# Performance work log

Hardware: AMD Instinct MI355X
Metric: run time of the kernel (lower is better)

## Reference

```python
import jax, jax.numpy as jnp
import numpy as np

B, S, D, H = 2, 2048, 1024, 16
HD = D // H  # head depth


def setup_inputs() -> dict:
    key = jax.random.key(0)
    ks = jax.random.split(key, 8)
    scale = 0.02
    K = jax.random.normal(ks[0], (B, S, D), jnp.float32)
    V = jax.random.normal(ks[1], (B, S, D), jnp.float32)
    Q = jax.random.normal(ks[2], (B, S, D), jnp.float32)
    # causal additive mask: 1.0 where attention is disallowed (strict upper triangle)
    mask = jnp.broadcast_to(
        jnp.triu(jnp.ones((S, S), jnp.float32), k=1)[None, None, :, :], (B, 1, S, S)
    )
    Wk = jax.random.normal(ks[3], (D, D), jnp.float32) * scale
    Wv = jax.random.normal(ks[4], (D, D), jnp.float32) * scale
    Wq = jax.random.normal(ks[5], (D, D), jnp.float32) * scale
    Wo = jax.random.normal(ks[6], (D, D), jnp.float32) * scale
    z = jnp.zeros((D,), jnp.float32)
    return {"K": K, "V": V, "Q": Q, "mask": mask,
            "Wk": Wk, "bk": z, "Wv": Wv, "bv": z,
            "Wq": Wq, "bq": z, "Wo": Wo, "bo": z}


def _split_heads(x):  # [B,S,D] -> [B,H,S,HD]
    return x.reshape(B, S, H, HD).transpose(0, 2, 1, 3)


def reference(K, V, Q, mask, Wk, bk, Wv, bv, Wq, bq, Wo, bo):
    k = _split_heads(K @ Wk + bk)
    v = _split_heads(V @ Wv + bv)
    q = _split_heads(Q @ Wq + bq)
    # NOTE: source scales by sqrt(d_model), not sqrt(head_depth)
    logits = jnp.einsum("bhqd,bhkd->bhqk", q, k) / jnp.sqrt(jnp.float32(D))
    logits = logits + mask * (-1e9)
    attn = jax.nn.softmax(logits, axis=-1)
    out = jnp.einsum("bhqk,bhkd->bhqd", attn, v)  # [B,H,S,HD]
    out = out.transpose(0, 2, 1, 3).reshape(B, S, D)
    return out @ Wo + bo
```

## Files before the change

kernel.cpp:

```cpp
#include <hip/hip_runtime.h>
#include <hip/hip_bf16.h>

typedef unsigned short u16;
typedef unsigned int u32;
typedef unsigned long long u64;
typedef __attribute__((ext_vector_type(8))) __bf16 bf16x8;
typedef __attribute__((ext_vector_type(4))) float f32x4;

#define SEQ 2048
#define DM 1024
#define NH 16
#define HDim 64

__device__ __forceinline__ float bf_lo(u32 u) { return __uint_as_float(u << 16); }
__device__ __forceinline__ float bf_hi(u32 u) { return __uint_as_float(u & 0xffff0000u); }
__device__ __forceinline__ u16 f2bf(float f) {
    u32 u = __float_as_uint(f);
    u32 r = (u + 0x7fffu + ((u >> 16) & 1u)) >> 16;
    return (u16)r;
}
__device__ __forceinline__ float bf2f(u16 h) { return __uint_as_float(((u32)h) << 16); }

#define GLD16(g, l)                                                         \
    __builtin_amdgcn_global_load_lds(                                       \
        (const __attribute__((address_space(1))) void*)(g),                 \
        (__attribute__((address_space(3))) void*)(l), 16, 0, 0)

__global__ __launch_bounds__(64)
void detect_dtype(const u32* __restrict__ q, int* __restrict__ flag)
{
    const int t = threadIdx.x;
    const u32 w = q[t];
    const int e0 = ((w & 0xffffu) >> 7) & 0xff;
    const int e1 = ((w >> 16) >> 7) & 0xff;
    const int big = (e0 >= 0x90 || e1 >= 0x90) ? 1 : 0;
    const unsigned long long b = __ballot(big);
    if (t == 0) *flag = (b != 0ull) ? 1 : 0;
}

__global__ __launch_bounds__(256)
void prep_x(const void* __restrict__ q, const void* __restrict__ k,
            const void* __restrict__ v, u16* __restrict__ dst,
            const int* __restrict__ flagp)
{
    const int z = blockIdx.z;
    const void* src = (z == 0) ? q : (z == 1) ? k : v;
    const size_t i0 = ((size_t)blockIdx.x * 256 + threadIdx.x) * 8;
    u16* d = dst + (size_t)z * 4194304 + i0;
    if (*flagp) {
        const uint4* s = reinterpret_cast<const uint4*>((const float*)src + i0);
        uint4 a = s[0], b = s[1];
        u16 o[8];
        o[0] = f2bf(__uint_as_float(a.x)); o[1] = f2bf(__uint_as_float(a.y));
        o[2] = f2bf(__uint_as_float(a.z)); o[3] = f2bf(__uint_as_float(a.w));
        o[4] = f2bf(__uint_as_float(b.x)); o[5] = f2bf(__uint_as_float(b.y));
        o[6] = f2bf(__uint_as_float(b.z)); o[7] = f2bf(__uint_as_float(b.w));
        *reinterpret_cast<uint4*>(d) = *reinterpret_cast<const uint4*>(o);
    } else {
        *reinterpret_cast<uint4*>(d) =
            *reinterpret_cast<const uint4*>((const u16*)src + i0);
    }
}

__global__ __launch_bounds__(256)
void transpose_w(const void* __restrict__ w0, const void* __restrict__ w1,
                 const void* __restrict__ w2, const void* __restrict__ w3,
                 u16* __restrict__ wt, const int* __restrict__ flagp)
{
    __shared__ u16 T[64 * 66];
    const int z = blockIdx.z;
    const void* src = (z == 0) ? w0 : (z == 1) ? w1 : (z == 2) ? w2 : w3;
    const int n0 = blockIdx.x * 64, k0 = blockIdx.y * 64;
    const int t = threadIdx.x;
    const int c = t & 63, g = t >> 6;
    const int f = *flagp;
    if (f) {
        const float* W = (const float*)src;
#pragma unroll
        for (int i = 0; i < 16; i++) {
            const int kl = g * 16 + i;
            T[kl * 66 + c] = f2bf(W[(size_t)(k0 + kl) * DM + n0 + c]);
        }
    } else {
        const u16* W = (const u16*)src;
#pragma unroll
        for (int i = 0; i < 16; i++) {
            const int kl = g * 16 + i;
            T[kl * 66 + c] = W[(size_t)(k0 + kl) * DM + n0 + c];
        }
    }
    __syncthreads();
    u16* dst = wt + (size_t)z * 1048576;
#pragma unroll
    for (int i = 0; i < 16; i++) {
        const int nl = g * 16 + i;
        dst[(size_t)(n0 + nl) * DM + k0 + c] = T[c * 66 + nl];
    }
}

__global__ __launch_bounds__(256)
void prep_bias(const void* __restrict__ b0, const void* __restrict__ b1,
               const void* __restrict__ b2, const void* __restrict__ b3,
               u16* __restrict__ dst, const int* __restrict__ flagp)
{
    const int t = threadIdx.x;
    const int f = *flagp;
#pragma unroll
    for (int j = 0; j < 16; j++) {
        const int idx = t * 16 + j;
        const int z = idx >> 10, e = idx & 1023;
        const void* src = (z == 0) ? b0 : (z == 1) ? b1 : (z == 2) ? b2 : b3;
        dst[idx] = f ? f2bf(((const float*)src)[e]) : ((const u16*)src)[e];
    }
}

__global__ __launch_bounds__(256)
void gemm128(const u16* __restrict__ Xall, const u16* __restrict__ Wtall,
             const u16* __restrict__ ball, u16* __restrict__ Yall,
             void* __restrict__ dout, int zbase, const int* __restrict__ flagp)
{
    __shared__ __align__(16) u16 As[128 * 32];
    __shared__ __align__(16) u16 Bs[128 * 32];

    const int zz = zbase + blockIdx.z;
    const u16* X  = Xall + ((zz == 3) ? 0 : (size_t)zz * 4194304);
    const u16* Wt = Wtall + (size_t)zz * 1048576;

    const int t    = threadIdx.x;
    const int w    = t >> 6;
    const int lane = t & 63;
    const int quad = lane >> 4;
    const int ln   = lane & 15;
    const int m0   = blockIdx.y * 128;
    const int n0   = blockIdx.x * 128;

    f32x4 acc[4][4];
#pragma unroll
    for (int i = 0; i < 4; i++)
#pragma unroll
        for (int j = 0; j < 4; j++) acc[i][j] = (f32x4){0.f, 0.f, 0.f, 0.f};

    const u16* ag = X  + (size_t)(m0 + w * 32 + (lane >> 2)) * DM + (lane & 3) * 8;
    const u16* bg = Wt + (size_t)(n0 + w * 32 + (lane >> 2)) * DM + (lane & 3) * 8;
    u16* al = &As[w * 1024];
    u16* bl = &Bs[w * 1024];

    const int wr = (w >> 1) * 64;
    const int wc = (w & 1) * 64;

    for (int kk = 0; kk < DM; kk += 32) {
        GLD16(ag,             al);
        GLD16(ag + 16 * DM,   al + 512);
        GLD16(bg,             bl);
        GLD16(bg + 16 * DM,   bl + 512);
        ag += 32; bg += 32;
        __syncthreads();

        bf16x8 af[4], bfr[4];
#pragma unroll
        for (int rt = 0; rt < 4; rt++)
            af[rt] = *reinterpret_cast<const bf16x8*>(&As[(wr + rt * 16 + ln) * 32 + quad * 8]);
#pragma unroll
        for (int ct = 0; ct < 4; ct++)
            bfr[ct] = *reinterpret_cast<const bf16x8*>(&Bs[(wc + ct * 16 + ln) * 32 + quad * 8]);
#pragma unroll
        for (int rt = 0; rt < 4; rt++)
#pragma unroll
            for (int ct = 0; ct < 4; ct++)
                acc[rt][ct] = __builtin_amdgcn_mfma_f32_16x16x32_bf16(
                    af[rt], bfr[ct], acc[rt][ct], 0, 0, 0);
        __syncthreads();
    }

    const int f = *flagp;
    const float scale = (zz == 0) ? 0.03125f : 1.0f;
    u16* Y = Yall + (size_t)zz * 4194304;

#pragma unroll
    for (int ct = 0; ct < 4; ct++) {
        const int n = n0 + wc + ct * 16 + ln;
        const float bv = bf2f(ball[zz * 1024 + n]);
        const int h = n >> 6, hd = n & (HDim - 1);
#pragma unroll
        for (int rt = 0; rt < 4; rt++) {
            const int m = m0 + wr + rt * 16 + quad * 4;
            if (zz == 2) {
                const int b = m >> 11, s = m & (SEQ - 1);
                u16 o4[4];
#pragma unroll
                for (int r = 0; r < 4; r++) o4[r] = f2bf(acc[rt][ct][r] + bv);
                *reinterpret_cast<u64*>(
                    Y + (((size_t)(b * NH + h) * HDim + hd) * SEQ + s)) =
                    *reinterpret_cast<const u64*>(o4);
            } else if (zz == 3) {
#pragma unroll
                for (int r = 0; r < 4; r++) {
                    const float val = acc[rt][ct][r] + bv;
                    if (f) ((float*)dout)[(size_t)(m + r) * DM + n] = val;
                    else   ((u16*)dout)[(size_t)(m + r) * DM + n] = f2bf(val);
                }
            } else {
#pragma unroll
                for (int r = 0; r < 4; r++) {
                    const int mm = m + r;
                    const int b = mm >> 11, s = mm & (SEQ - 1);
                    Y[(((size_t)(b * NH + h)) * SEQ + s) * HDim + hd] =
                        f2bf((acc[rt][ct][r] + bv) * scale);
                }
            }
        }
    }
}

__global__ __launch_bounds__(256)
void attn_mfma(const u16* __restrict__ qh, const u16* __restrict__ kh,
               const u16* __restrict__ vt, u16* __restrict__ ctx)
{
    __shared__ __align__(16) u16 Ks[64 * 72];
    __shared__ __align__(16) u16 Vs[64 * 72];
    __shared__ __align__(16) u16 Ps[64 * 72];

    const int t    = threadIdx.x;
    const int qt   = blockIdx.x;
    const int bh   = blockIdx.y;
    const int w    = t >> 6;
    const int lane = t & 63;
    const int quad = lane >> 4;
    const int ln   = lane & 15;

    const size_t kbase = (size_t)bh * SEQ * HDim;
    const size_t vbase = (size_t)bh * HDim * SEQ;

    const u16* qrow = qh + kbase + (size_t)(qt * 64 + w * 16 + ln) * HDim;
    const bf16x8 qf0 = *reinterpret_cast<const bf16x8*>(qrow + quad * 8);
    const bf16x8 qf1 = *reinterpret_cast<const bf16x8*>(qrow + 32 + quad * 8);

    f32x4 o[4];
#pragma unroll
    for (int i = 0; i < 4; i++) o[i] = (f32x4){0.f, 0.f, 0.f, 0.f};
    float lsum[4] = {0.f, 0.f, 0.f, 0.f};

    const int srow = t >> 2;
    const int sc   = (t & 3) * 16;
    const int myrow = qt * 64 + w * 16 + quad * 4;
    const int ntiles = qt + 1;

    for (int kt = 0; kt < ntiles; kt++) {
        {
            const uint4* ks = reinterpret_cast<const uint4*>(
                kh + kbase + (size_t)(kt * 64 + srow) * HDim + sc);
            uint4* kd = reinterpret_cast<uint4*>(&Ks[srow * 72 + sc]);
            kd[0] = ks[0];
            kd[1] = ks[1];
            const uint4* vs = reinterpret_cast<const uint4*>(
                vt + vbase + (size_t)srow * SEQ + kt * 64 + sc);
            uint4* vd = reinterpret_cast<uint4*>(&Vs[srow * 72 + sc]);
            vd[0] = vs[0];
            vd[1] = vs[1];
        }
        __syncthreads();

        f32x4 s[4];
#pragma unroll
        for (int ct = 0; ct < 4; ct++) {
            const u16* kr = &Ks[(ct * 16 + ln) * 72 + quad * 8];
            bf16x8 kf0 = *reinterpret_cast<const bf16x8*>(kr);
            bf16x8 kf1 = *reinterpret_cast<const bf16x8*>(kr + 32);
            f32x4 z = (f32x4){0.f, 0.f, 0.f, 0.f};
            z = __builtin_amdgcn_mfma_f32_16x16x32_bf16(qf0, kf0, z, 0, 0, 0);
            s[ct] = __builtin_amdgcn_mfma_f32_16x16x32_bf16(qf1, kf1, z, 0, 0, 0);
        }

#pragma unroll
        for (int ct = 0; ct < 4; ct++) {
            const int kcol = kt * 64 + ct * 16 + ln;
#pragma unroll
            for (int r = 0; r < 4; r++) {
                const float e = (kcol <= myrow + r) ? __expf(s[ct][r]) : 0.f;
                lsum[r] += e;
                Ps[(w * 16 + quad * 4 + r) * 72 + ct * 16 + ln] = f2bf(e);
            }
        }

#pragma unroll
        for (int ks = 0; ks < 2; ks++) {
            bf16x8 pf = *reinterpret_cast<const bf16x8*>(
                &Ps[(w * 16 + ln) * 72 + ks * 32 + quad * 8]);
#pragma unroll
            for (int nt = 0; nt < 4; nt++) {
                bf16x8 vf = *reinterpret_cast<const bf16x8*>(
                    &Vs[(nt * 16 + ln) * 72 + ks * 32 + quad * 8]);
                o[nt] = __builtin_amdgcn_mfma_f32_16x16x32_bf16(pf, vf, o[nt], 0, 0, 0);
            }
        }
        __syncthreads();
    }

#pragma unroll
    for (int m = 1; m < 16; m <<= 1) {
#pragma unroll
        for (int r = 0; r < 4; r++) lsum[r] += __shfl_xor(lsum[r], m);
    }
    float inv[4];
#pragma unroll
    for (int r = 0; r < 4; r++) inv[r] = 1.f / lsum[r];

    const int b = bh >> 4;
    const int h = bh & 15;
#pragma unroll
    for (int r = 0; r < 4; r++) {
        const int srow_g = qt * 64 + w * 16 + quad * 4 + r;
        u16* dst = ctx + ((size_t)(b * SEQ + srow_g)) * DM + h * HDim + ln;
#pragma unroll
        for (int nt = 0; nt < 4; nt++)
            dst[nt * 16] = f2bf(o[nt][r] * inv[r]);
    }
}

__global__ __launch_bounds__(256)
void gemm_bias(const void* __restrict__ Xv, const void* __restrict__ Wv,
               const void* __restrict__ biasv, void* __restrict__ Yv,
               int M, int N, int K, int mode, int xsel, int wsel, int ysel,
               float scale, const int* __restrict__ flagp)
{
    __shared__ __align__(16) u16 As[64 * 32];
    __shared__ __align__(16) u16 Bs[64 * 40];

    const int f  = *flagp;
    const bool xf = (xsel != 0) && (f != 0);
    const bool wf = (wsel != 0) && (f != 0);
    const bool yf = (ysel != 0) && (f != 0);

    const u16*   Xb = (const u16*)Xv;
    const float* Xf = (const float*)Xv;
    const u16*   Wb = (const u16*)Wv;
    const float* Wf = (const float*)Wv;

    const int t    = threadIdx.x;
    const int m0   = blockIdx.y * 64;
    const int n0   = blockIdx.x * 64;
    const int w    = t >> 6;
    const int lane = t & 63;
    const int quad = lane >> 4;
    const int ln   = lane & 15;

    f32x4 acc[4];
#pragma unroll
    for (int i = 0; i < 4; i++) acc[i] = (f32x4){0.f, 0.f, 0.f, 0.f};

    const int a_row = t >> 2;
    const int a_c8  = (t & 3) * 8;
    const int b_n   = t & 63;
    const int b_k8  = (t >> 6) * 8;

    for (int kk = 0; kk < K; kk += 32) {
        const size_t aoff = (size_t)(m0 + a_row) * K + kk + a_c8;
        if (!xf) {
            *reinterpret_cast<uint4*>(&As[a_row * 32 + a_c8]) =
                *reinterpret_cast<const uint4*>(Xb + aoff);
        } else {
            const float* src = Xf + aoff;
            uint4 u0 = reinterpret_cast<const uint4*>(src)[0];
            uint4 u1 = reinterpret_cast<const uint4*>(src)[1];
            u16 tmp[8];
            tmp[0] = f2bf(__uint_as_float(u0.x));
            tmp[1] = f2bf(__uint_as_float(u0.y));
            tmp[2] = f2bf(__uint_as_float(u0.z));
            tmp[3] = f2bf(__uint_as_float(u0.w));
            tmp[4] = f2bf(__uint_as_float(u1.x));
            tmp[5] = f2bf(__uint_as_float(u1.y));
            tmp[6] = f2bf(__uint_as_float(u1.z));
            tmp[7] = f2bf(__uint_as_float(u1.w));
            *reinterpret_cast<uint4*>(&As[a_row * 32 + a_c8]) =
                *reinterpret_cast<const uint4*>(tmp);
        }
        u16 tmp[8];
        if (!wf) {
#pragma unroll
            for (int j = 0; j < 8; j++)
                tmp[j] = Wb[(size_t)(kk + b_k8 + j) * N + n0 + b_n];
        } else {
#pragma unroll
            for (int j = 0; j < 8; j++)
                tmp[j] = f2bf(Wf[(size_t)(kk + b_k8 + j) * N + n0 + b_n]);
        }
        *reinterpret_cast<uint4*>(&Bs[b_n * 40 + b_k8]) =
            *reinterpret_cast<const uint4*>(tmp);

        __syncthreads();

        bf16x8 bfrag = *reinterpret_cast<const bf16x8*>(&Bs[(w * 16 + ln) * 40 + quad * 8]);
#pragma unroll
        for (int rt = 0; rt < 4; rt++) {
            bf16x8 afrag = *reinterpret_cast<const bf16x8*>(&As[(rt * 16 + ln) * 32 + quad * 8]);
            acc[rt] = __builtin_amdgcn_mfma_f32_16x16x32_bf16(afrag, bfrag, acc[rt], 0, 0, 0);
        }
        __syncthreads();
    }

    const int n = n0 + w * 16 + ln;
    const float bv = wf ? ((const float*)biasv)[n] : bf2f(((const u16*)biasv)[n]);
#pragma unroll
    for (int rt = 0; rt < 4; rt++) {
        if (mode == 2) {
            const int m = m0 + rt * 16 + quad * 4;
            const int b = m >> 11;
            const int s = m & (SEQ - 1);
            const int h = n >> 6;
            const int hd = n & (HDim - 1);
            u16 o4[4];
#pragma unroll
            for (int r = 0; r < 4; r++) o4[r] = f2bf((acc[rt][r] + bv) * scale);
            *reinterpret_cast<u64*>(
                (u16*)Yv + (((size_t)(b * NH + h) * HDim + hd) * SEQ + s)) =
                *reinterpret_cast<const u64*>(o4);
        } else {
#pragma unroll
            for (int r = 0; r < 4; r++) {
                const int m = m0 + rt * 16 + quad * 4 + r;
                const float val = (acc[rt][r] + bv) * scale;
                if (mode == 0) {
                    if (yf) ((float*)Yv)[(size_t)m * N + n] = val;
                    else    ((u16*)Yv)[(size_t)m * N + n] = f2bf(val);
                } else {
                    const int b = m >> 11;
                    const int s = m & (SEQ - 1);
                    const int h = n >> 6;
                    const int hd = n & (HDim - 1);
                    ((u16*)Yv)[(((size_t)(b * NH + h)) * SEQ + s) * HDim + hd] = f2bf(val);
                }
            }
        }
    }
}

extern "C" void kernel_launch(void* const* d_in, const int* in_sizes, int n_in,
                              void* d_out, int out_size, void* d_ws, size_t ws_size,
                              hipStream_t stream)
{
    const void* Kin = d_in[0];
    const void* Vin = d_in[1];
    const void* Qin = d_in[2];
    const void* Wk = d_in[4];
    const void* bk = d_in[5];
    const void* Wv = d_in[6];
    const void* bv = d_in[7];
    const void* Wq = d_in[8];
    const void* bq = d_in[9];
    const void* Wo = d_in[10];
    const void* bo = d_in[11];

    char* ws = (char*)d_ws;

    const size_t NEED = ((size_t)29360128 + 4096) * 2 + 256;

    if (ws_size >= NEED) {
        u16* Xall  = (u16*)ws;
        u16* Yall  = (u16*)ws + 12582912;
        u16* Wtall = (u16*)ws + 25165824;
        u16* ball  = (u16*)ws + 29360128;
        int* flag  = (int*)((u16*)ws + 29364224);
        u16* qhp   = Yall;
        u16* khp   = Yall + 4194304;
        u16* vtp   = Yall + 8388608;
        u16* ctx   = Xall;

        hipLaunchKernelGGL(detect_dtype, dim3(1), dim3(64), 0, stream,
                           (const u32*)Qin, flag);
        hipLaunchKernelGGL(prep_x, dim3(2048, 1, 3), dim3(256), 0, stream,
                           Qin, Kin, Vin, Xall, flag);
        hipLaunchKernelGGL(transpose_w, dim3(16, 16, 4), dim3(256), 0, stream,
                           Wq, Wk, Wv, Wo, Wtall, flag);
        hipLaunchKernelGGL(prep_bias, dim3(1), dim3(256), 0, stream,
                           bq, bk, bv, bo, ball, flag);

        hipLaunchKernelGGL(gemm128, dim3(8, 32, 3), dim3(256), 0, stream,
                           Xall, Wtall, ball, Yall, (void*)0, 0, flag);

        hipLaunchKernelGGL(attn_mfma, dim3(SEQ / 64, 2 * NH), dim3(256), 0,
                           stream, qhp, khp, vtp, ctx);

        hipLaunchKernelGGL(gemm128, dim3(8, 32, 1), dim3(256), 0, stream,
                           Xall, Wtall, ball, Yall, d_out, 3, flag);
    } else {
        const size_t SEG = (size_t)2 * SEQ * DM * sizeof(u16);
        u16* qh  = (u16*)(ws);
        u16* khd = (u16*)(ws + SEG);
        u16* vtd = (u16*)(ws + 2 * SEG);
        u16* ctx = (u16*)(ws + 3 * SEG);
        int* flag = (int*)(ws + 4 * SEG);

        hipLaunchKernelGGL(detect_dtype, dim3(1), dim3(64), 0, stream,
                           (const u32*)Qin, flag);

        const int M = 2 * SEQ;
        dim3 ggrid(DM / 64, M / 64);
        dim3 gblk(256);

        hipLaunchKernelGGL(gemm_bias, ggrid, gblk, 0, stream, Qin, Wq, bq, qh,  M, DM, DM, 1, 1, 1, 0, 0.03125f, flag);
        hipLaunchKernelGGL(gemm_bias, ggrid, gblk, 0, stream, Kin, Wk, bk, khd, M, DM, DM, 1, 1, 1, 0, 1.0f,     flag);
        hipLaunchKernelGGL(gemm_bias, ggrid, gblk, 0, stream, Vin, Wv, bv, vtd, M, DM, DM, 2, 1, 1, 0, 1.0f,     flag);

        hipLaunchKernelGGL(attn_mfma, dim3(SEQ / 64, 2 * NH), dim3(256), 0,
                           stream, qh, khd, vtd, ctx);

        hipLaunchKernelGGL(gemm_bias, ggrid, gblk, 0, stream, ctx, Wo, bo, d_out, M, DM, DM, 0, 0, 1, 1, 1.0f, flag);
    }
}
```

Baseline: 302.7 us.

## Pair causal query tiles per attention block, fuse prep kernels, vectorize QK epilogue

Each attention block now handles two query tiles, i and 31-i, and shares one K/V tile load between them. This balances the triangular causal work across blocks and halves the grid. The four preprocessing kernels (dtype detect, input convert, weight transpose, bias) are merged into one launch, and the dtype check is recomputed inline rather than read from a flag. The Q/K projection GEMM swaps its MFMA operands so the epilogue can write 4 contiguous head-dim elements per store. In exchange, the attention kernel holds two accumulators per block, which raises register pressure.

```diff
diff --git a/kernel.cpp b/kernel.cpp
--- a/kernel.cpp
+++ b/kernel.cpp
@@ -26,103 +26,99 @@
         (const __attribute__((address_space(1))) void*)(g),                 \
         (__attribute__((address_space(3))) void*)(l), 16, 0, 0)
 
-__global__ __launch_bounds__(64)
-void detect_dtype(const u32* __restrict__ q, int* __restrict__ flag)
-{
+__device__ __forceinline__ bool detect_f32(const u32* q)
+{
+    const u32 w = q[threadIdx.x & 63];
+    const int e0 = ((w & 0xffffu) >> 7) & 0xff;
+    const int e1 = (w >> 23) & 0xff;
+    const unsigned long long b = __ballot(e0 >= 0x90 || e1 >= 0x90);
+    return b != 0ull;
+}
+
+__global__ __launch_bounds__(256)
+void prep_all(const void* __restrict__ Qin, const void* __restrict__ Kin,
+              const void* __restrict__ Vin,
+              const void* __restrict__ w0, const void* __restrict__ w1,
+              const void* __restrict__ w2, const void* __restrict__ w3,
+              const void* __restrict__ b0, const void* __restrict__ b1,
+              const void* __restrict__ b2, const void* __restrict__ b3,
+              u16* __restrict__ Xall, u16* __restrict__ Wtall,
+              u16* __restrict__ ball)
+{
+    __shared__ u16 T[64 * 66];
+    const bool f = detect_f32((const u32*)Qin);
     const int t = threadIdx.x;
-    const u32 w = q[t];
-    const int e0 = ((w & 0xffffu) >> 7) & 0xff;
-    const int e1 = ((w >> 16) >> 7) & 0xff;
-    const int big = (e0 >= 0x90 || e1 >= 0x90) ? 1 : 0;
-    const unsigned long long b = __ballot(big);
-    if (t == 0) *flag = (b != 0ull) ? 1 : 0;
-}
-
-__global__ __launch_bounds__(256)
-void prep_x(const void* __restrict__ q, const void* __restrict__ k,
-            const void* __restrict__ v, u16* __restrict__ dst,
-            const int* __restrict__ flagp)
-{
-    const int z = blockIdx.z;
-    const void* src = (z == 0) ? q : (z == 1) ? k : v;
-    const size_t i0 = ((size_t)blockIdx.x * 256 + threadIdx.x) * 8;
-    u16* d = dst + (size_t)z * 4194304 + i0;
-    if (*flagp) {
-        const uint4* s = reinterpret_cast<const uint4*>((const float*)src + i0);
-        uint4 a = s[0], b = s[1];
-        u16 o[8];
-        o[0] = f2bf(__uint_as_float(a.x)); o[1] = f2bf(__uint_as_float(a.y));
-        o[2] = f2bf(__uint_as_float(a.z)); o[3] = f2bf(__uint_as_float(a.w));
-        o[4] = f2bf(__uint_as_float(b.x)); o[5] = f2bf(__uint_as_float(b.y));
-        o[6] = f2bf(__uint_as_float(b.z)); o[7] = f2bf(__uint_as_float(b.w));
-        *reinterpret_cast<uint4*>(d) = *reinterpret_cast<const uint4*>(o);
+    const int bid = blockIdx.x;
+
+    if (bid < 6144) {
+        const int z = bid >> 11;
+        const int bx = bid & 2047;
+        const void* src = (z == 0) ? Qin : (z == 1) ? Kin : Vin;
+        const size_t i0 = ((size_t)bx * 256 + t) * 8;
+        u16* d = Xall + (size_t)z * 4194304 + i0;
+        if (f) {
+            const uint4* s = reinterpret_cast<const uint4*>((const float*)src + i0);
+            uint4 a = s[0], b = s[1];
+            u16 o[8];
+            o[0] = f2bf(__uint_as_float(a.x)); o[1] = f2bf(__uint_as_float(a.y));
+            o[2] = f2bf(__uint_as_float(a.z)); o[3] = f2bf(__uint_as_float(a.w));
+            o[4] = f2bf(__uint_as_float(b.x)); o[5] = f2bf(__uint_as_float(b.y));
+            o[6] = f2bf(__uint_as_float(b.z)); o[7] = f2bf(__uint_as_float(b.w));
+            *reinterpret_cast<uint4*>(d) = *reinterpret_cast<const uint4*>(o);
+        } else {
+            *reinterpret_cast<uint4*>(d) =
+                *reinterpret_cast<const uint4*>((const u16*)src + i0);
+        }
+    } else if (bid < 7168) {
+        const int r = bid - 6144;
+        const int z = r >> 8;
+        const void* src = (z == 0) ? w0 : (z == 1) ? w1 : (z == 2) ? w2 : w3;
+        const int n0 = ((r >> 4) & 15) * 64;
+        const int k0 = (r & 15) * 64;
+        const int c = t & 63, g = t >> 6;
+        if (f) {
+            const float* W = (const float*)src;
+#pragma unroll
+            for (int i = 0; i < 16; i++) {
+                const int kl = g * 16 + i;
+                T[kl * 66 + c] = f2bf(W[(size_t)(k0 + kl) * DM + n0 + c]);
+            }
+        } else {
+            const u16* W = (const u16*)src;
+#pragma unroll
+            for (int i = 0; i < 16; i++) {
+                const int kl = g * 16 + i;
+                T[kl * 66 + c] = W[(size_t)(k0 + kl) * DM + n0 + c];
+            }
+        }
+        __syncthreads();
+        u16* dst = Wtall + (size_t)z * 1048576;
+#pragma unroll
+        for (int i = 0; i < 16; i++) {
+            const int nl = g * 16 + i;
+            dst[(size_t)(n0 + nl) * DM + k0 + c] = T[c * 66 + nl];
+        }
     } else {
-        *reinterpret_cast<uint4*>(d) =
-            *reinterpret_cast<const uint4*>((const u16*)src + i0);
-    }
-}
-
-__global__ __launch_bounds__(256)
-void transpose_w(const void* __restrict__ w0, const void* __restrict__ w1,
-                 const void* __restrict__ w2, const void* __restrict__ w3,
-                 u16* __restrict__ wt, const int* __restrict__ flagp)
-{
-    __shared__ u16 T[64 * 66];
-    const int z = blockIdx.z;
-    const void* src = (z == 0) ? w0 : (z == 1) ? w1 : (z == 2) ? w2 : w3;
-    const int n0 = blockIdx.x * 64, k0 = blockIdx.y * 64;
-    const int t = threadIdx.x;
-    const int c = t & 63, g = t >> 6;
-    const int f = *flagp;
-    if (f) {
-        const float* W = (const float*)src;
-#pragma unroll
-        for (int i = 0; i < 16; i++) {
-            const int kl = g * 16 + i;
-            T[kl * 66 + c] = f2bf(W[(size_t)(k0 + kl) * DM + n0 + c]);
-        }
-    } else {
-        const u16* W = (const u16*)src;
-#pragma unroll
-        for (int i = 0; i < 16; i++) {
-            const int kl = g * 16 + i;
-            T[kl * 66 + c] = W[(size_t)(k0 + kl) * DM + n0 + c];
-        }
-    }
-    __syncthreads();
-    u16* dst = wt + (size_t)z * 1048576;
-#pragma unroll
-    for (int i = 0; i < 16; i++) {
-        const int nl = g * 16 + i;
-        dst[(size_t)(n0 + nl) * DM + k0 + c] = T[c * 66 + nl];
-    }
-}
-
-__global__ __launch_bounds__(256)
-void prep_bias(const void* __restrict__ b0, const void* __restrict__ b1,
-               const void* __restrict__ b2, const void* __restrict__ b3,
-               u16* __restrict__ dst, const int* __restrict__ flagp)
-{
-    const int t = threadIdx.x;
-    const int f = *flagp;
-#pragma unroll
-    for (int j = 0; j < 16; j++) {
-        const int idx = t * 16 + j;
-        const int z = idx >> 10, e = idx & 1023;
-        const void* src = (z == 0) ? b0 : (z == 1) ? b1 : (z == 2) ? b2 : b3;
-        dst[idx] = f ? f2bf(((const float*)src)[e]) : ((const u16*)src)[e];
+#pragma unroll
+        for (int j = 0; j < 16; j++) {
+            const int idx = t * 16 + j;
+            const int z = idx >> 10, e = idx & 1023;
+            const void* src = (z == 0) ? b0 : (z == 1) ? b1 : (z == 2) ? b2 : b3;
+            ball[idx] = f ? f2bf(((const float*)src)[e]) : ((const u16*)src)[e];
+        }
     }
 }
 
 __global__ __launch_bounds__(256)
 void gemm128(const u16* __restrict__ Xall, const u16* __restrict__ Wtall,
              const u16* __restrict__ ball, u16* __restrict__ Yall,
-             void* __restrict__ dout, int zbase, const int* __restrict__ flagp)
+             void* __restrict__ dout, int zbase, const u32* __restrict__ qdet)
 {
     __shared__ __align__(16) u16 As[128 * 32];
     __shared__ __align__(16) u16 Bs[128 * 32];
 
     const int zz = zbase + blockIdx.z;
+    const bool swp = (zz == 0) || (zz == 1);
     const u16* X  = Xall + ((zz == 3) ? 0 : (size_t)zz * 4194304);
     const u16* Wt = Wtall + (size_t)zz * 1048576;
 
@@ -149,10 +145,10 @@
     const int wc = (w & 1) * 64;
 
     for (int kk = 0; kk < DM; kk += 32) {
-        GLD16(ag,             al);
-        GLD16(ag + 16 * DM,   al + 512);
-        GLD16(bg,             bl);
-        GLD16(bg + 16 * DM,   bl + 512);
+        GLD16(ag,           al);
+        GLD16(ag + 16 * DM, al + 512);
+        GLD16(bg,           bl);
+        GLD16(bg + 16 * DM, bl + 512);
         ag += 32; bg += 32;
         __syncthreads();
 
@@ -163,28 +159,57 @@
 #pragma unroll
         for (int ct = 0; ct < 4; ct++)
             bfr[ct] = *reinterpret_cast<const bf16x8*>(&Bs[(wc + ct * 16 + ln) * 32 + quad * 8]);
-#pragma unroll
-        for (int rt = 0; rt < 4; rt++)
-#pragma unroll
-            for (int ct = 0; ct < 4; ct++)
-                acc[rt][ct] = __builtin_amdgcn_mfma_f32_16x16x32_bf16(
-                    af[rt], bfr[ct], acc[rt][ct], 0, 0, 0);
-        __syncthreads();
-    }
-
-    const int f = *flagp;
-    const float scale = (zz == 0) ? 0.03125f : 1.0f;
+        if (swp) {
+#pragma unroll
+            for (int rt = 0; rt < 4; rt++)
+#pragma unroll
+                for (int ct = 0; ct < 4; ct++)
+                    acc[rt][ct] = __builtin_amdgcn_mfma_f32_16x16x32_bf16(
+                        bfr[ct], af[rt], acc[rt][ct], 0, 0, 0);
+        } else {
+#pragma unroll
+            for (int rt = 0; rt < 4; rt++)
+#pragma unroll
+                for (int ct = 0; ct < 4; ct++)
+                    acc[rt][ct] = __builtin_amdgcn_mfma_f32_16x16x32_bf16(
+                        af[rt], bfr[ct], acc[rt][ct], 0, 0, 0);
+        }
+        __syncthreads();
+    }
+
     u16* Y = Yall + (size_t)zz * 4194304;
 
-#pragma unroll
-    for (int ct = 0; ct < 4; ct++) {
-        const int n = n0 + wc + ct * 16 + ln;
-        const float bv = bf2f(ball[zz * 1024 + n]);
-        const int h = n >> 6, hd = n & (HDim - 1);
-#pragma unroll
-        for (int rt = 0; rt < 4; rt++) {
-            const int m = m0 + wr + rt * 16 + quad * 4;
-            if (zz == 2) {
+    if (swp) {
+        const float scale = (zz == 0) ? 0.03125f : 1.0f;
+#pragma unroll
+        for (int ct = 0; ct < 4; ct++) {
+            const int nb = n0 + wc + ct * 16 + quad * 4;
+            const int h = nb >> 6, hd = nb & (HDim - 1);
+            float bv[4];
+#pragma unroll
+            for (int r = 0; r < 4; r++) bv[r] = bf2f(ball[zz * 1024 + nb + r]);
+#pragma unroll
+            for (int rt = 0; rt < 4; rt++) {
+                const int m = m0 + wr + rt * 16 + ln;
+                const int b = m >> 11, s = m & (SEQ - 1);
+                u16 o4[4];
+#pragma unroll
+                for (int r = 0; r < 4; r++)
+                    o4[r] = f2bf((acc[rt][ct][r] + bv[r]) * scale);
+                *reinterpret_cast<u64*>(
+                    Y + (((size_t)(b * NH + h)) * SEQ + s) * HDim + hd) =
+                    *reinterpret_cast<const u64*>(o4);
+            }
+        }
+    } else if (zz == 2) {
+#pragma unroll
+        for (int ct = 0; ct < 4; ct++) {
+            const int n = n0 + wc + ct * 16 + ln;
+            const float bv = bf2f(ball[zz * 1024 + n]);
+            const int h = n >> 6, hd = n & (HDim - 1);
+#pragma unroll
+            for (int rt = 0; rt < 4; rt++) {
+                const int m = m0 + wr + rt * 16 + quad * 4;
                 const int b = m >> 11, s = m & (SEQ - 1);
                 u16 o4[4];
 #pragma unroll
@@ -192,22 +217,64 @@
                 *reinterpret_cast<u64*>(
                     Y + (((size_t)(b * NH + h) * HDim + hd) * SEQ + s)) =
                     *reinterpret_cast<const u64*>(o4);
-            } else if (zz == 3) {
+            }
+        }
+    } else {
+        const bool f = detect_f32(qdet);
+#pragma unroll
+        for (int ct = 0; ct < 4; ct++) {
+            const int n = n0 + wc + ct * 16 + ln;
+            const float bv = bf2f(ball[zz * 1024 + n]);
+#pragma unroll
+            for (int rt = 0; rt < 4; rt++) {
+                const int m = m0 + wr + rt * 16 + quad * 4;
 #pragma unroll
                 for (int r = 0; r < 4; r++) {
                     const float val = acc[rt][ct][r] + bv;
                     if (f) ((float*)dout)[(size_t)(m + r) * DM + n] = val;
                     else   ((u16*)dout)[(size_t)(m + r) * DM + n] = f2bf(val);
                 }
-            } else {
-#pragma unroll
-                for (int r = 0; r < 4; r++) {
-                    const int mm = m + r;
-                    const int b = mm >> 11, s = mm & (SEQ - 1);
-                    Y[(((size_t)(b * NH + h)) * SEQ + s) * HDim + hd] =
-                        f2bf((acc[rt][ct][r] + bv) * scale);
-                }
             }
+        }
+    }
+}
+
+struct AttnAcc { f32x4 o[4]; float l[4]; };
+
+__device__ __forceinline__ void attn_tile(
+    const u16* __restrict__ Ks, const u16* __restrict__ Vs,
+    u16* __restrict__ Ps, const bf16x8& qf0, const bf16x8& qf1,
+    int kt, int rowb, int w, int quad, int ln, AttnAcc& a)
+{
+    f32x4 s[4];
+#pragma unroll
+    for (int ct = 0; ct < 4; ct++) {
+        const u16* kr = &Ks[(ct * 16 + ln) * 72 + quad * 8];
+        bf16x8 kf0 = *reinterpret_cast<const bf16x8*>(kr);
+        bf16x8 kf1 = *reinterpret_cast<const bf16x8*>(kr + 32);
+        f32x4 z = (f32x4){0.f, 0.f, 0.f, 0.f};
+        z = __builtin_amdgcn_mfma_f32_16x16x32_bf16(qf0, kf0, z, 0, 0, 0);
+        s[ct] = __builtin_amdgcn_mfma_f32_16x16x32_bf16(qf1, kf1, z, 0, 0, 0);
+    }
+#pragma unroll
+    for (int ct = 0; ct < 4; ct++) {
+        const int kcol = kt * 64 + ct * 16 + ln;
+#pragma unroll
+        for (int r = 0; r < 4; r++) {
+            const float e = (kcol <= rowb + r) ? __expf(s[ct][r]) : 0.f;
+            a.l[r] += e;
+            Ps[(w * 16 + quad * 4 + r) * 68 + ct * 16 + ln] = f2bf(e);
+        }
+    }
+#pragma unroll
+    for (int ks = 0; ks < 2; ks++) {
+        bf16x8 pf = *reinterpret_cast<const bf16x8*>(
+            &Ps[(w * 16 + ln) * 68 + ks * 32 + quad * 8]);
+#pragma unroll
+        for (int nt = 0; nt < 4; nt++) {
+            bf16x8 vf = *reinterpret_cast<const bf16x8*>(
+                &Vs[(nt * 16 + ln) * 72 + ks * 32 + quad * 8]);
+            a.o[nt] = __builtin_amdgcn_mfma_f32_16x16x32_bf16(pf, vf, a.o[nt], 0, 0, 0);
         }
     }
 }
@@ -218,34 +285,41 @@
 {
     __shared__ __align__(16) u16 Ks[64 * 72];
     __shared__ __align__(16) u16 Vs[64 * 72];
-    __shared__ __align__(16) u16 Ps[64 * 72];
+    __shared__ __align__(16) u16 Ps[64 * 68];
 
     const int t    = threadIdx.x;
-    const int qt   = blockIdx.x;
+    const int i    = blockIdx.x;
     const int bh   = blockIdx.y;
     const int w    = t >> 6;
     const int lane = t & 63;
     const int quad = lane >> 4;
     const int ln   = lane & 15;
+    const int qtH  = 31 - i;
+    const int qtL  = i;
 
     const size_t kbase = (size_t)bh * SEQ * HDim;
     const size_t vbase = (size_t)bh * HDim * SEQ;
 
-    const u16* qrow = qh + kbase + (size_t)(qt * 64 + w * 16 + ln) * HDim;
-    const bf16x8 qf0 = *reinterpret_cast<const bf16x8*>(qrow + quad * 8);
-    const bf16x8 qf1 = *reinterpret_cast<const bf16x8*>(qrow + 32 + quad * 8);
-
-    f32x4 o[4];
-#pragma unroll
-    for (int i = 0; i < 4; i++) o[i] = (f32x4){0.f, 0.f, 0.f, 0.f};
-    float lsum[4] = {0.f, 0.f, 0.f, 0.f};
+    const u16* qrH = qh + kbase + (size_t)(qtH * 64 + w * 16 + ln) * HDim;
+    const bf16x8 qfH0 = *reinterpret_cast<const bf16x8*>(qrH + quad * 8);
+    const bf16x8 qfH1 = *reinterpret_cast<const bf16x8*>(qrH + 32 + quad * 8);
+    const u16* qrL = qh + kbase + (size_t)(qtL * 64 + w * 16 + ln) * HDim;
+    const bf16x8 qfL0 = *reinterpret_cast<const bf16x8*>(qrL + quad * 8);
+    const bf16x8 qfL1 = *reinterpret_cast<const bf16x8*>(qrL + 32 + quad * 8);
+
+    AttnAcc aH, aL;
+#pragma unroll
+    for (int k = 0; k < 4; k++) {
+        aH.o[k] = (f32x4){0.f, 0.f, 0.f, 0.f}; aH.l[k] = 0.f;
+        aL.o[k] = (f32x4){0.f, 0.f, 0.f, 0.f}; aL.l[k] = 0.f;
+    }
 
     const int srow = t >> 2;
     const int sc   = (t & 3) * 16;
-    const int myrow = qt * 64 + w * 16 + quad * 4;
-    const int ntiles = qt + 1;
-
-    for (int kt = 0; kt < ntiles; kt++) {
+    const int rowHb = qtH * 64 + w * 16 + quad * 4;
+    const int rowLb = qtL * 64 + w * 16 + quad * 4;
+
+    for (int kt = 0; kt <= qtH; kt++) {
         {
             const uint4* ks = reinterpret_cast<const uint4*>(
                 kh + kbase + (size_t)(kt * 64 + srow) * HDim + sc);
@@ -260,61 +334,49 @@
         }
         __syncthreads();
 
-        f32x4 s[4];
-#pragma unroll
-        for (int ct = 0; ct < 4; ct++) {
-            const u16* kr = &Ks[(ct * 16 + ln) * 72 + quad * 8];
-            bf16x8 kf0 = *reinterpret_cast<const bf16x8*>(kr);
-            bf16x8 kf1 = *reinterpret_cast<const bf16x8*>(kr + 32);
-            f32x4 z = (f32x4){0.f, 0.f, 0.f, 0.f};
-            z = __builtin_amdgcn_mfma_f32_16x16x32_bf16(qf0, kf0, z, 0, 0, 0);
-            s[ct] = __builtin_amdgcn_mfma_f32_16x16x32_bf16(qf1, kf1, z, 0, 0, 0);
-        }
-
-#pragma unroll
-        for (int ct = 0; ct < 4; ct++) {
-            const int kcol = kt * 64 + ct * 16 + ln;
-#pragma unroll
-            for (int r = 0; r < 4; r++) {
-                const float e = (kcol <= myrow + r) ? __expf(s[ct][r]) : 0.f;
-                lsum[r] += e;
-                Ps[(w * 16 + quad * 4 + r) * 72 + ct * 16 + ln] = f2bf(e);
-            }
-        }
-
-#pragma unroll
-        for (int ks = 0; ks < 2; ks++) {
-            bf16x8 pf = *reinterpret_cast<const bf16x8*>(
-                &Ps[(w * 16 + ln) * 72 + ks * 32 + quad * 8]);
-#pragma unroll
-            for (int nt = 0; nt < 4; nt++) {
-                bf16x8 vf = *reinterpret_cast<const bf16x8*>(
-                    &Vs[(nt * 16 + ln) * 72 + ks * 32 + quad * 8]);
-                o[nt] = __builtin_amdgcn_mfma_f32_16x16x32_bf16(pf, vf, o[nt], 0, 0, 0);
-            }
-        }
+        attn_tile(Ks, Vs, Ps, qfH0, qfH1, kt, rowHb, w, quad, ln, aH);
+        if (kt <= qtL)
+            attn_tile(Ks, Vs, Ps, qfL0, qfL1, kt, rowLb, w, quad, ln, aL);
+
         __syncthreads();
     }
 
 #pragma unroll
     for (int m = 1; m < 16; m <<= 1) {
 #pragma unroll
-        for (int r = 0; r < 4; r++) lsum[r] += __shfl_xor(lsum[r], m);
-    }
-    float inv[4];
-#pragma unroll
-    for (int r = 0; r < 4; r++) inv[r] = 1.f / lsum[r];
+        for (int r = 0; r < 4; r++) {
+            aH.l[r] += __shfl_xor(aH.l[r], m);
+            aL.l[r] += __shfl_xor(aL.l[r], m);
+        }
+    }
 
     const int b = bh >> 4;
     const int h = bh & 15;
 #pragma unroll
     for (int r = 0; r < 4; r++) {
-        const int srow_g = qt * 64 + w * 16 + quad * 4 + r;
-        u16* dst = ctx + ((size_t)(b * SEQ + srow_g)) * DM + h * HDim + ln;
-#pragma unroll
-        for (int nt = 0; nt < 4; nt++)
-            dst[nt * 16] = f2bf(o[nt][r] * inv[r]);
-    }
+        const float invH = 1.f / aH.l[r];
+        const float invL = 1.f / aL.l[r];
+        const int sH = qtH * 64 + w * 16 + quad * 4 + r;
+        const int sL = qtL * 64 + w * 16 + quad * 4 + r;
+        u16* dH = ctx + ((size_t)(b * SEQ + sH)) * DM + h * HDim + ln;
+        u16* dL = ctx + ((size_t)(b * SEQ + sL)) * DM + h * HDim + ln;
+#pragma unroll
+        for (int nt = 0; nt < 4; nt++) {
+            dH[nt * 16] = f2bf(aH.o[nt][r] * invH);
+            dL[nt * 16] = f2bf(aL.o[nt][r] * invL);
+        }
+    }
+}
+
+__global__ __launch_bounds__(64)
+void detect_dtype(const u32* __restrict__ q, int* __restrict__ flag)
+{
+    const int t = threadIdx.x;
+    const u32 w = q[t];
+    const int e0 = ((w & 0xffffu) >> 7) & 0xff;
+    const int e1 = (w >> 23) & 0xff;
+    const unsigned long long b = __ballot(e0 >= 0x90 || e1 >= 0x90);
+    if (t == 0) *flag = (b != 0ull) ? 1 : 0;
 }
 
 __global__ __launch_bounds__(256)
@@ -451,7 +513,6 @@
     const void* bo = d_in[11];
 
     char* ws = (char*)d_ws;
-
     const size_t NEED = ((size_t)29360128 + 4096) * 2 + 256;
 
     if (ws_size >= NEED) {
@@ -459,29 +520,23 @@
         u16* Yall  = (u16*)ws + 12582912;
         u16* Wtall = (u16*)ws + 25165824;
         u16* ball  = (u16*)ws + 29360128;
-        int* flag  = (int*)((u16*)ws + 29364224);
         u16* qhp   = Yall;
         u16* khp   = Yall + 4194304;
         u16* vtp   = Yall + 8388608;
         u16* ctx   = Xall;
 
-        hipLaunchKernelGGL(detect_dtype, dim3(1), dim3(64), 0, stream,
-                           (const u32*)Qin, flag);
-        hipLaunchKernelGGL(prep_x, dim3(2048, 1, 3), dim3(256), 0, stream,
-                           Qin, Kin, Vin, Xall, flag);
-        hipLaunchKernelGGL(transpose_w, dim3(16, 16, 4), dim3(256), 0, stream,
-                           Wq, Wk, Wv, Wo, Wtall, flag);
-        hipLaunchKernelGGL(prep_bias, dim3(1), dim3(256), 0, stream,
-                           bq, bk, bv, bo, ball, flag);
+        hipLaunchKernelGGL(prep_all, dim3(7169), dim3(256), 0, stream,
+                           Qin, Kin, Vin, Wq, Wk, Wv, Wo, bq, bk, bv, bo,
+                           Xall, Wtall, ball);
 
         hipLaunchKernelGGL(gemm128, dim3(8, 32, 3), dim3(256), 0, stream,
-                           Xall, Wtall, ball, Yall, (void*)0, 0, flag);
-
-        hipLaunchKernelGGL(attn_mfma, dim3(SEQ / 64, 2 * NH), dim3(256), 0,
+                           Xall, Wtall, ball, Yall, (void*)0, 0, (const u32*)Qin);
+
+        hipLaunchKernelGGL(attn_mfma, dim3(16, 2 * NH), dim3(256), 0,
                            stream, qhp, khp, vtp, ctx);
 
         hipLaunchKernelGGL(gemm128, dim3(8, 32, 1), dim3(256), 0, stream,
-                           Xall, Wtall, ball, Yall, d_out, 3, flag);
+                           Xall, Wtall, ball, Yall, d_out, 3, (const u32*)Qin);
     } else {
         const size_t SEG = (size_t)2 * SEQ * DM * sizeof(u16);
         u16* qh  = (u16*)(ws);
@@ -501,7 +556,7 @@
         hipLaunchKernelGGL(gemm_bias, ggrid, gblk, 0, stream, Kin, Wk, bk, khd, M, DM, DM, 1, 1, 1, 0, 1.0f,     flag);
         hipLaunchKernelGGL(gemm_bias, ggrid, gblk, 0, stream, Vin, Wv, bv, vtd, M, DM, DM, 2, 1, 1, 0, 1.0f,     flag);
 
-        hipLaunchKernelGGL(attn_mfma, dim3(SEQ / 64, 2 * NH), dim3(256), 0,
+        hipLaunchKernelGGL(attn_mfma, dim3(16, 2 * NH), dim3(256), 0,
                            stream, qh, khd, vtd, ctx);
 
         hipLaunchKernelGGL(gemm_bias, ggrid, gblk, 0, stream, ctx, Wo, bo, d_out, M, DM, DM, 0, 0, 1, 1, 1.0f, flag);
```

Result: faster. 281.0 us (-7.1%).
